# Optimization experiments

Hardware: AMD Instinct MI355X
Metric: run time of the kernel (lower is better)

Reference implementation:

```python
import jax, jax.numpy as jnp
import numpy as np

TAU = 1.0            # module's self.temperature (set externally in the repo)
NUM_EMBED = 1024     # num_embeddings
EPS = 1e-10


def setup_inputs() -> dict:
    key = jax.random.key(0)
    k1, k2, k3 = jax.random.split(key, 3)
    B, S, N, D = 8, 2048, 1024, 512
    logits = jax.random.normal(k1, (B, S, N), dtype=jnp.float32)
    # uniform samples for deterministic gumbel noise g = -log(-log(u))
    u = jax.random.uniform(k2, (B, S, N), dtype=jnp.float32,
                           minval=1e-6, maxval=1.0 - 1e-6)
    embed = jax.random.normal(k3, (N, D), dtype=jnp.float32) * 0.02
    return {"logits": logits, "u": u, "embed": embed}


def reference(logits, u, embed):
    # F.gumbel_softmax(logits, tau, dim=2, hard=True)
    gumbel = -jnp.log(-jnp.log(u))                      # [B,S,N]
    y_soft = jax.nn.softmax((logits + gumbel) / TAU, axis=2)
    ind = jnp.argmax(y_soft, axis=2)                    # [B,S] int
    y_hard = jax.nn.one_hot(ind, logits.shape[2], dtype=y_soft.dtype)
    # straight-through: hard value, soft gradient
    one_hot = y_hard + y_soft - jax.lax.stop_gradient(y_soft)
    # einsum('b s n, n d -> b s d') with the codebook
    z_q = jnp.einsum('bsn,nd->bsd', one_hot, embed)     # [B,S,D]
    qy = jax.nn.softmax(logits, axis=2)
    diff = -jnp.log(qy * NUM_EMBED + EPS) / qy          # [B,S,N]
    return z_q, diff, ind
```

## Files before the change

### kernel.cpp

```cpp
#include <hip/hip_runtime.h>
#include <math.h>

#define N_EMB 1024
#define D_EMB 512

__global__ __launch_bounds__(256) void gumbel_quantize_kernel(
    const float* __restrict__ logits,
    const float* __restrict__ u,
    const float* __restrict__ embed,
    float*       __restrict__ zq,
    float*       __restrict__ diff,
    float*       __restrict__ indf)
{
    const int lane = threadIdx.x & 63;
    const int wave = threadIdx.x >> 6;
    const int row  = blockIdx.x * 4 + wave;
    const size_t rbase = (size_t)row * N_EMB;

    const float4* lp = (const float4*)(logits + rbase);
    const float4* up = (const float4*)(u      + rbase);

    float4 l4[4], u4[4];
    #pragma unroll
    for (int c = 0; c < 4; ++c) l4[c] = lp[c * 64 + lane];
    #pragma unroll
    for (int c = 0; c < 4; ++c) u4[c] = up[c * 64 + lane];

    float lv[16];
    #pragma unroll
    for (int c = 0; c < 4; ++c) {
        lv[c*4+0] = l4[c].x; lv[c*4+1] = l4[c].y;
        lv[c*4+2] = l4[c].z; lv[c*4+3] = l4[c].w;
    }

    float smax = -INFINITY; int sidx = 0;
    float lmax = -INFINITY;
    #pragma unroll
    for (int c = 0; c < 4; ++c) {
        const float us[4] = {u4[c].x, u4[c].y, u4[c].z, u4[c].w};
        #pragma unroll
        for (int j = 0; j < 4; ++j) {
            const float g  = -logf(-logf(us[j]));
            const float sc = lv[c*4+j] + g;
            const int idx  = c * 256 + lane * 4 + j;
            if (sc > smax) { smax = sc; sidx = idx; }
            lmax = fmaxf(lmax, lv[c*4+j]);
        }
    }

    #pragma unroll
    for (int off = 32; off > 0; off >>= 1) {
        const float v2 = __shfl_xor(smax, off, 64);
        const int   i2 = __shfl_xor(sidx, off, 64);
        if (v2 > smax || (v2 == smax && i2 < sidx)) { smax = v2; sidx = i2; }
        lmax = fmaxf(lmax, __shfl_xor(lmax, off, 64));
    }
    const int   ind = sidx;
    const float m   = lmax;

    float e[16];
    float psum = 0.f;
    #pragma unroll
    for (int j = 0; j < 16; ++j) { e[j] = __expf(lv[j] - m); psum += e[j]; }
    #pragma unroll
    for (int off = 32; off > 0; off >>= 1) psum += __shfl_xor(psum, off, 64);
    const float sum = psum;
    const float inv = 1.0f / sum;
    const float L = logf((float)N_EMB * inv);

    float4* dp = (float4*)(diff + rbase);
    #pragma unroll
    for (int c = 0; c < 4; ++c) {
        float d[4];
        #pragma unroll
        for (int j = 0; j < 4; ++j) {
            const int k = c * 4 + j;
            d[j] = -((lv[k] - m) + L) * sum * __builtin_amdgcn_rcpf(e[k]);
        }
        dp[c * 64 + lane] = make_float4(d[0], d[1], d[2], d[3]);
    }

    const float4* erow = (const float4*)(embed + (size_t)ind * D_EMB);
    float4*       zrow = (float4*)(zq + (size_t)row * D_EMB);
    #pragma unroll
    for (int c = 0; c < 2; ++c) zrow[c * 64 + lane] = erow[c * 64 + lane];

    if (lane == 0) indf[row] = (float)ind;
}

extern "C" void kernel_launch(void* const* d_in, const int* in_sizes, int n_in,
                              void* d_out, int out_size, void* d_ws, size_t ws_size,
                              hipStream_t stream) {
    const float* logits = (const float*)d_in[0];
    const float* u      = (const float*)d_in[1];
    const float* embed  = (const float*)d_in[2];

    const int rows = in_sizes[0] / N_EMB;

    float* out  = (float*)d_out;
    float* zq   = out;
    float* diff = zq + (size_t)rows * D_EMB;
    float* indf = diff + (size_t)rows * N_EMB;

    gumbel_quantize_kernel<<<rows / 4, 256, 0, stream>>>(logits, u, embed,
                                                         zq, diff, indf);
}
```

Before: 206.4 us.

## Process two rows per wave with upfront loads and nontemporal stores

Each wave now handles two rows, spaced half the grid apart, and issues all loads for both rows before computing, so more memory requests are in flight per wave. Outputs (diff, z_q, indices) are written with nontemporal stores to avoid polluting the cache. The diff formula now recomputes exp(m-l) instead of a reciprocal of a stored exp, and uses log(N) - log(sum). The cost is higher register pressure and half as many waves.

```diff
diff --git a/kernel.cpp b/kernel.cpp
--- a/kernel.cpp
+++ b/kernel.cpp
@@ -3,6 +3,9 @@
 
 #define N_EMB 1024
 #define D_EMB 512
+#define LN_N  6.9314718056f
+
+typedef float f32x4 __attribute__((ext_vector_type(4)));
 
 __global__ __launch_bounds__(256) void gumbel_quantize_kernel(
     const float* __restrict__ logits,
@@ -10,82 +13,100 @@
     const float* __restrict__ embed,
     float*       __restrict__ zq,
     float*       __restrict__ diff,
-    float*       __restrict__ indf)
+    float*       __restrict__ indf,
+    int waves_total)
 {
     const int lane = threadIdx.x & 63;
     const int wave = threadIdx.x >> 6;
-    const int row  = blockIdx.x * 4 + wave;
-    const size_t rbase = (size_t)row * N_EMB;
+    const int wid  = blockIdx.x * 4 + wave;
 
-    const float4* lp = (const float4*)(logits + rbase);
-    const float4* up = (const float4*)(u      + rbase);
+    const int r0 = wid;
+    const int r1 = wid + waves_total;
 
-    float4 l4[4], u4[4];
-    #pragma unroll
-    for (int c = 0; c < 4; ++c) l4[c] = lp[c * 64 + lane];
-    #pragma unroll
-    for (int c = 0; c < 4; ++c) u4[c] = up[c * 64 + lane];
-
-    float lv[16];
-    #pragma unroll
-    for (int c = 0; c < 4; ++c) {
-        lv[c*4+0] = l4[c].x; lv[c*4+1] = l4[c].y;
-        lv[c*4+2] = l4[c].z; lv[c*4+3] = l4[c].w;
-    }
-
-    float smax = -INFINITY; int sidx = 0;
-    float lmax = -INFINITY;
-    #pragma unroll
-    for (int c = 0; c < 4; ++c) {
-        const float us[4] = {u4[c].x, u4[c].y, u4[c].z, u4[c].w};
+    f32x4 l4[2][4], u4[2][4];
+    {
+        const f32x4* lp0 = (const f32x4*)(logits + (size_t)r0 * N_EMB);
+        const f32x4* up0 = (const f32x4*)(u      + (size_t)r0 * N_EMB);
+        const f32x4* lp1 = (const f32x4*)(logits + (size_t)r1 * N_EMB);
+        const f32x4* up1 = (const f32x4*)(u      + (size_t)r1 * N_EMB);
         #pragma unroll
-        for (int j = 0; j < 4; ++j) {
-            const float g  = -logf(-logf(us[j]));
-            const float sc = lv[c*4+j] + g;
-            const int idx  = c * 256 + lane * 4 + j;
-            if (sc > smax) { smax = sc; sidx = idx; }
-            lmax = fmaxf(lmax, lv[c*4+j]);
-        }
+        for (int c = 0; c < 4; ++c) l4[0][c] = lp0[c * 64 + lane];
+        #pragma unroll
+        for (int c = 0; c < 4; ++c) u4[0][c] = up0[c * 64 + lane];
+        #pragma unroll
+        for (int c = 0; c < 4; ++c) l4[1][c] = lp1[c * 64 + lane];
+        #pragma unroll
+        for (int c = 0; c < 4; ++c) u4[1][c] = up1[c * 64 + lane];
     }
 
     #pragma unroll
-    for (int off = 32; off > 0; off >>= 1) {
-        const float v2 = __shfl_xor(smax, off, 64);
-        const int   i2 = __shfl_xor(sidx, off, 64);
-        if (v2 > smax || (v2 == smax && i2 < sidx)) { smax = v2; sidx = i2; }
-        lmax = fmaxf(lmax, __shfl_xor(lmax, off, 64));
+    for (int p = 0; p < 2; ++p) {
+        const int row = (p == 0) ? r0 : r1;
+        const size_t rbase = (size_t)row * N_EMB;
+
+        float lv[16], uv[16];
+        #pragma unroll
+        for (int c = 0; c < 4; ++c) {
+            #pragma unroll
+            for (int j = 0; j < 4; ++j) {
+                lv[c*4+j] = l4[p][c][j];
+                uv[c*4+j] = u4[p][c][j];
+            }
+        }
+
+        float smax = -INFINITY; int sidx = 0;
+        float lmax = -INFINITY;
+        #pragma unroll
+        for (int c = 0; c < 4; ++c) {
+            #pragma unroll
+            for (int j = 0; j < 4; ++j) {
+                const int k = c * 4 + j;
+                const float g  = -logf(-logf(uv[k]));
+                const float sc = lv[k] + g;
+                const int idx  = c * 256 + lane * 4 + j;
+                if (sc > smax) { smax = sc; sidx = idx; }
+                lmax = fmaxf(lmax, lv[k]);
+            }
+        }
+
+        #pragma unroll
+        for (int off = 32; off > 0; off >>= 1) {
+            const float v2 = __shfl_xor(smax, off, 64);
+            const int   i2 = __shfl_xor(sidx, off, 64);
+            if (v2 > smax || (v2 == smax && i2 < sidx)) { smax = v2; sidx = i2; }
+            lmax = fmaxf(lmax, __shfl_xor(lmax, off, 64));
+        }
+        const int   ind = sidx;
+        const float m   = lmax;
+
+        float psum = 0.f;
+        #pragma unroll
+        for (int j = 0; j < 16; ++j) psum += __expf(lv[j] - m);
+        #pragma unroll
+        for (int off = 32; off > 0; off >>= 1) psum += __shfl_xor(psum, off, 64);
+        const float sum = psum;
+        const float L   = LN_N - logf(sum);
+
+        f32x4* dp = (f32x4*)(diff + rbase);
+        #pragma unroll
+        for (int c = 0; c < 4; ++c) {
+            f32x4 d;
+            #pragma unroll
+            for (int j = 0; j < 4; ++j) {
+                const int k = c * 4 + j;
+                d[j] = -((lv[k] - m) + L) * sum * __expf(m - lv[k]);
+            }
+            __builtin_nontemporal_store(d, dp + c * 64 + lane);
+        }
+
+        const f32x4* erow = (const f32x4*)(embed + (size_t)ind * D_EMB);
+        f32x4*       zrow = (f32x4*)(zq + (size_t)row * D_EMB);
+        #pragma unroll
+        for (int c = 0; c < 2; ++c)
+            __builtin_nontemporal_store(erow[c * 64 + lane], zrow + c * 64 + lane);
+
+        if (lane == 0) __builtin_nontemporal_store((float)ind, indf + row);
     }
-    const int   ind = sidx;
-    const float m   = lmax;
-
-    float e[16];
-    float psum = 0.f;
-    #pragma unroll
-    for (int j = 0; j < 16; ++j) { e[j] = __expf(lv[j] - m); psum += e[j]; }
-    #pragma unroll
-    for (int off = 32; off > 0; off >>= 1) psum += __shfl_xor(psum, off, 64);
-    const float sum = psum;
-    const float inv = 1.0f / sum;
-    const float L = logf((float)N_EMB * inv);
-
-    float4* dp = (float4*)(diff + rbase);
-    #pragma unroll
-    for (int c = 0; c < 4; ++c) {
-        float d[4];
-        #pragma unroll
-        for (int j = 0; j < 4; ++j) {
-            const int k = c * 4 + j;
-            d[j] = -((lv[k] - m) + L) * sum * __builtin_amdgcn_rcpf(e[k]);
-        }
-        dp[c * 64 + lane] = make_float4(d[0], d[1], d[2], d[3]);
-    }
-
-    const float4* erow = (const float4*)(embed + (size_t)ind * D_EMB);
-    float4*       zrow = (float4*)(zq + (size_t)row * D_EMB);
-    #pragma unroll
-    for (int c = 0; c < 2; ++c) zrow[c * 64 + lane] = erow[c * 64 + lane];
-
-    if (lane == 0) indf[row] = (float)ind;
 }
 
 extern "C" void kernel_launch(void* const* d_in, const int* in_sizes, int n_in,
@@ -102,6 +123,10 @@
     float* diff = zq + (size_t)rows * D_EMB;
     float* indf = diff + (size_t)rows * N_EMB;
 
-    gumbel_quantize_kernel<<<rows / 4, 256, 0, stream>>>(logits, u, embed,
-                                                         zq, diff, indf);
+    const int waves_total = rows / 2;
+    const int blocks      = waves_total / 4;
+
+    gumbel_quantize_kernel<<<blocks, 256, 0, stream>>>(logits, u, embed,
+                                                       zq, diff, indf,
+                                                       waves_total);
 }
```

Result: no change. 208.1 us (+0.8%).
